# Optimization experiments

Measured on AMD Instinct MI355X. Metric: run time of the kernel, lower is better.

Reference implementation:

```python
import jax, jax.numpy as jnp
import numpy as np

N = 50000      # nodes
E = 400000     # edges
F_IN = 128     # num_features
HID = 64       # hidden_channels
HEADS = 4      # num_heads
HEADC = HID // HEADS  # 16
C = 10         # num_classes
K_HOPS = 2     # K
CST = 1e-05


def setup_inputs() -> dict:
    key = jax.random.key(0)
    ks = jax.random.split(key, 12)
    def lin(k, out_dim, in_dim):
        return jax.random.normal(k, (out_dim, in_dim), jnp.float32) / np.sqrt(in_dim).astype(np.float32)
    return {
        "node_feat": jax.random.normal(ks[0], (N, F_IN), jnp.float32),
        "edge_index": jax.random.randint(ks[1], (2, E), 0, N, jnp.int64),
        "W_in": lin(ks[2], HID, F_IN),   "b_in": jnp.zeros((HID,), jnp.float32),
        "W_q": lin(ks[3], HEADS * HEADC, HID), "b_q": jnp.zeros((HEADS * HEADC,), jnp.float32),
        "W_k": lin(ks[4], HEADS * HEADC, HID), "b_k": jnp.zeros((HEADS * HEADC,), jnp.float32),
        "W_v": lin(ks[5], HEADS * C, HID),     "b_v": jnp.zeros((HEADS * C,), jnp.float32),
        "W_out": lin(ks[6], C, HEADS * C),     "b_out": jnp.zeros((C,), jnp.float32),
        "hopwise": jnp.ones((K_HOPS + 1,), jnp.float32),
        "headwise": jnp.zeros((HEADS, K_HOPS), jnp.float32),
    }


def reference(node_feat, edge_index, W_in, b_in, W_q, b_q, W_k, b_k, W_v, b_v,
              W_out, b_out, hopwise, headwise):
    # input transform (dropout is identity in eval mode)
    x = jax.nn.relu(node_feat @ W_in.T + b_in)                       # [N, HID]
    Q = (1.0 + jax.nn.elu(x @ W_q.T + b_q)).reshape(N, HEADS, HEADC)  # [N,H,hc]
    Kf = (1.0 + jax.nn.elu(x @ W_k.T + b_k)).reshape(N, HEADS, HEADC)
    V = (x @ W_v.T + b_v).reshape(N, HEADS, C)                        # [N,H,C]

    M = jnp.einsum('nhi,nhj->nhij', Kf, V)                            # [N,H,hc,C]
    hidden = V * hopwise[0]                                           # gamma_softmax path
    layerwise = jax.nn.softmax(headwise, axis=0)                      # softmax over heads

    row, col = edge_index[0], edge_index[1]
    for hop in range(K_HOPS):
        # propM / propK: sum-aggregate source features into targets
        M = jax.ops.segment_sum(M[row], col, num_segments=N)
        Kf = jax.ops.segment_sum(Kf[row], col, num_segments=N)
        H = jnp.einsum('nhi,nhij->nhj', Q, M)                         # [N,H,C]
        Cd = jnp.einsum('nhi,nhi->nh', Q, Kf)[..., None] + CST        # [N,H,1]
        gamma = hopwise[hop + 1] * layerwise[:, hop][:, None]         # [H,1]
        hidden = hidden + gamma * (H / Cd)

    # multi_concat output projection
    out = hidden.reshape(N, HEADS * C) @ W_out.T + b_out              # [N,C]
    return out
```

## Files before the change

kernel.cpp:

```cpp
#include <hip/hip_runtime.h>
#include <hip/hip_bf16.h>

#define N_NODES 50000
#define N_EDGES 400000
#define F_IN    128
#define HID     64
#define HEADS   4
#define HEADC   16
#define C_CLS   10
#define HC      (HEADS * C_CLS)
#define CST     1e-5f

#define WIN_OFF 0
#define WQ_OFF  1024
#define WK_OFF  1536
#define WV_OFF  2048
#define WB_TOT  2432

typedef short bf16x8 __attribute__((ext_vector_type(8)));
typedef float f32x4  __attribute__((ext_vector_type(4)));
typedef float floatx2 __attribute__((ext_vector_type(2)));

__device__ __forceinline__ unsigned pack_bf16x2(float a, float b) {
    union { __hip_bfloat162 h2; unsigned u; } cv;
    cv.h2.x = __float2bfloat16(a);
    cv.h2.y = __float2bfloat16(b);
    return cv.u;
}
__device__ __forceinline__ float2 bf2_to_f2(unsigned u) {
    union { unsigned x; float f; } a, b;
    a.x = u << 16;
    b.x = u & 0xffff0000u;
    return make_float2(a.f, b.f);
}
union FragU { uint4 u; bf16x8 b; };
__device__ __forceinline__ bf16x8 ldfrag(const uint4* p) { FragU f; f.u = *p; return f.b; }
__device__ __forceinline__ bf16x8 pack8(const float4& a0, const float4& a1) {
    FragU f;
    f.u.x = pack_bf16x2(a0.x, a0.y);
    f.u.y = pack_bf16x2(a0.z, a0.w);
    f.u.z = pack_bf16x2(a1.x, a1.y);
    f.u.w = pack_bf16x2(a1.z, a1.w);
    return f.b;
}
__device__ __forceinline__ void acc_edge_fp8(float kf, uint4 v, float* accM) {
    floatx2 f;
    f = __builtin_amdgcn_cvt_pk_f32_fp8(v.x, false); accM[0] += kf * f[0]; accM[1] += kf * f[1];
    f = __builtin_amdgcn_cvt_pk_f32_fp8(v.x, true);  accM[2] += kf * f[0]; accM[3] += kf * f[1];
    f = __builtin_amdgcn_cvt_pk_f32_fp8(v.y, false); accM[4] += kf * f[0]; accM[5] += kf * f[1];
    f = __builtin_amdgcn_cvt_pk_f32_fp8(v.y, true);  accM[6] += kf * f[0]; accM[7] += kf * f[1];
    f = __builtin_amdgcn_cvt_pk_f32_fp8(v.z, false); accM[8] += kf * f[0]; accM[9] += kf * f[1];
}

__global__ __launch_bounds__(256) void prep_kernel(
    const float* __restrict__ W_in, const float* __restrict__ W_q,
    const float* __restrict__ W_k,  const float* __restrict__ W_v,
    uint4* __restrict__ WB)
{
    const int idx = blockIdx.x * 256 + threadIdx.x;
    if (idx >= WB_TOT) return;
    const int lane = idx & 63;
    const int c = lane & 15, g = lane >> 4;
    const float* src = nullptr;
    if (idx < WQ_OFF) {
        const int f = idx >> 6, nt = f >> 2, kt = f & 3;
        src = W_in + (size_t)(nt * 16 + c) * F_IN + kt * 32 + g * 8;
    } else if (idx < WK_OFF) {
        const int f = (idx - WQ_OFF) >> 6, nt = f >> 1, kt = f & 1;
        src = W_q + (size_t)(nt * 16 + c) * HID + kt * 32 + g * 8;
    } else if (idx < WV_OFF) {
        const int f = (idx - WK_OFF) >> 6, nt = f >> 1, kt = f & 1;
        src = W_k + (size_t)(nt * 16 + c) * HID + kt * 32 + g * 8;
    } else {
        const int f = (idx - WV_OFF) >> 6, nt = f >> 1, kt = f & 1;
        const int row = nt * 16 + c;
        src = (row < HC) ? (W_v + (size_t)row * HID + kt * 32 + g * 8) : nullptr;
    }
    float v[8];
    #pragma unroll
    for (int j = 0; j < 8; ++j) v[j] = src ? src[j] : 0.0f;
    uint4 o;
    o.x = pack_bf16x2(v[0], v[1]);
    o.y = pack_bf16x2(v[2], v[3]);
    o.z = pack_bf16x2(v[4], v[5]);
    o.w = pack_bf16x2(v[6], v[7]);
    WB[idx] = o;
}

__global__ __launch_bounds__(256) void proj_kernel(
    const float* __restrict__ feat, const uint4* __restrict__ WB,
    const float* __restrict__ b_in, const float* __restrict__ b_q,
    const float* __restrict__ b_k,  const float* __restrict__ b_v,
    float* __restrict__ Q, __hip_bfloat16* __restrict__ Kf0,
    __hip_bfloat16* __restrict__ V0p)
{
    const int w = threadIdx.x >> 6;
    const int l = threadIdx.x & 63;
    const int c = l & 15, g = l >> 4;
    const int nb = blockIdx.x * 64 + w * 16;
    __shared__ float xs[4][16][68];

    f32x4 acc[4];
    #pragma unroll
    for (int nt = 0; nt < 4; ++nt) acc[nt] = (f32x4){0.f, 0.f, 0.f, 0.f};
    int arow = nb + c; if (arow >= N_NODES) arow = N_NODES - 1;
    const float* fbase = feat + (size_t)arow * F_IN + g * 8;
    #pragma unroll
    for (int kt = 0; kt < 4; ++kt) {
        const float4 a0 = *(const float4*)(fbase + kt * 32);
        const float4 a1 = *(const float4*)(fbase + kt * 32 + 4);
        const bf16x8 af = pack8(a0, a1);
        #pragma unroll
        for (int nt = 0; nt < 4; ++nt)
            acc[nt] = __builtin_amdgcn_mfma_f32_16x16x32_bf16(
                af, ldfrag(WB + WIN_OFF + (nt * 4 + kt) * 64 + l), acc[nt], 0, 0, 0);
    }
    #pragma unroll
    for (int nt = 0; nt < 4; ++nt) {
        const int col = nt * 16 + c;
        const float bi = b_in[col];
        #pragma unroll
        for (int i = 0; i < 4; ++i)
            xs[w][g * 4 + i][col] = fmaxf(acc[nt][i] + bi, 0.f);
    }
    __syncthreads();

    f32x4 qa[4], ka[4], va[3];
    #pragma unroll
    for (int nt = 0; nt < 4; ++nt) { qa[nt] = (f32x4){0.f,0.f,0.f,0.f}; ka[nt] = qa[nt]; }
    #pragma unroll
    for (int nt = 0; nt < 3; ++nt) va[nt] = (f32x4){0.f,0.f,0.f,0.f};
    #pragma unroll
    for (int kt = 0; kt < 2; ++kt) {
        const float* xr = &xs[w][c][kt * 32 + g * 8];
        const float4 x0 = *(const float4*)xr;
        const float4 x1 = *(const float4*)(xr + 4);
        const bf16x8 af = pack8(x0, x1);
        #pragma unroll
        for (int nt = 0; nt < 4; ++nt) {
            qa[nt] = __builtin_amdgcn_mfma_f32_16x16x32_bf16(
                af, ldfrag(WB + WQ_OFF + (nt * 2 + kt) * 64 + l), qa[nt], 0, 0, 0);
            ka[nt] = __builtin_amdgcn_mfma_f32_16x16x32_bf16(
                af, ldfrag(WB + WK_OFF + (nt * 2 + kt) * 64 + l), ka[nt], 0, 0, 0);
        }
        #pragma unroll
        for (int nt = 0; nt < 3; ++nt)
            va[nt] = __builtin_amdgcn_mfma_f32_16x16x32_bf16(
                af, ldfrag(WB + WV_OFF + (nt * 2 + kt) * 64 + l), va[nt], 0, 0, 0);
    }

    #pragma unroll
    for (int nt = 0; nt < 4; ++nt) {
        const int col = nt * 16 + c;
        const float bq = b_q[col], bk = b_k[col];
        #pragma unroll
        for (int i = 0; i < 4; ++i) {
            const int node = nb + g * 4 + i;
            if (node < N_NODES) {
                const float zq = qa[nt][i] + bq;
                Q[(size_t)node * HID + col] = (zq > 0.f) ? (zq + 1.f) : expf(zq);
                const float zk = ka[nt][i] + bk;
                Kf0[(size_t)node * HID + col] =
                    __float2bfloat16((zk > 0.f) ? (zk + 1.f) : expf(zk));
            }
        }
    }
    #pragma unroll
    for (int nt = 0; nt < 3; ++nt) {
        const int col = nt * 16 + c;
        if (col < HC) {
            const int hh = col / C_CLS, jj = col - hh * C_CLS;
            const float bv = b_v[col];
            #pragma unroll
            for (int i = 0; i < 4; ++i) {
                const int node = nb + g * 4 + i;
                if (node < N_NODES)
                    V0p[(size_t)node * 64 + hh * 16 + jj] = __float2bfloat16(va[nt][i] + bv);
            }
        }
    }
}

__global__ __launch_bounds__(256) void vconv_kernel(
    const __hip_bfloat16* __restrict__ V0p, uint4* __restrict__ V0f)
{
    const int t = blockIdx.x * 256 + threadIdx.x;
    if (t >= N_NODES * 4) return;
    const uint4* src = (const uint4*)V0p + (size_t)t * 2;
    const uint4 a = src[0];
    const unsigned b0 = ((const unsigned*)(src + 1))[0];
    float v[10];
    float2 f;
    f = bf2_to_f2(a.x); v[0] = f.x; v[1] = f.y;
    f = bf2_to_f2(a.y); v[2] = f.x; v[3] = f.y;
    f = bf2_to_f2(a.z); v[4] = f.x; v[5] = f.y;
    f = bf2_to_f2(a.w); v[6] = f.x; v[7] = f.y;
    f = bf2_to_f2(b0);  v[8] = f.x; v[9] = f.y;
    int d0 = 0, d1 = 0, d2 = 0;
    d0 = __builtin_amdgcn_cvt_pk_fp8_f32(v[0], v[1], d0, false);
    d0 = __builtin_amdgcn_cvt_pk_fp8_f32(v[2], v[3], d0, true);
    d1 = __builtin_amdgcn_cvt_pk_fp8_f32(v[4], v[5], d1, false);
    d1 = __builtin_amdgcn_cvt_pk_fp8_f32(v[6], v[7], d1, true);
    d2 = __builtin_amdgcn_cvt_pk_fp8_f32(v[8], v[9], d2, false);
    uint4 o;
    o.x = (unsigned)d0; o.y = (unsigned)d1; o.z = (unsigned)d2; o.w = 0u;
    V0f[t] = o;
}

__global__ __launch_bounds__(256) void hist_kernel(
    const int* __restrict__ ecol, int* __restrict__ deg)
{
    const int e = blockIdx.x * 256 + threadIdx.x;
    if (e < N_EDGES) atomicAdd(&deg[ecol[e]], 1);
}

__global__ __launch_bounds__(256) void offsets_kernel(
    const int* __restrict__ deg, int* __restrict__ rowptr,
    int* __restrict__ cursor, int* __restrict__ gcount)
{
    const int t    = threadIdx.x;
    const int lane = t & 63;
    const int wid  = t >> 6;
    const int n    = blockIdx.x * 256 + t;
    const int d    = (n < N_NODES) ? deg[n] : 0;

    int x = d;
    #pragma unroll
    for (int off = 1; off < 64; off <<= 1) {
        int v = __shfl_up(x, off);
        x += (lane >= off) ? v : 0;
    }

    __shared__ int wsum[4];
    __shared__ int wbase[4];
    __shared__ int bbase;
    if (lane == 63) wsum[wid] = x;
    __syncthreads();
    if (t == 0) {
        int b = 0;
        #pragma unroll
        for (int w = 0; w < 4; ++w) { wbase[w] = b; b += wsum[w]; }
        bbase = atomicAdd(gcount, b);
    }
    __syncthreads();

    if (n < N_NODES) {
        const int excl = bbase + wbase[wid] + (x - d);
        rowptr[n] = excl;
        cursor[n] = excl;
    }
}

__global__ __launch_bounds__(256) void scatter_kernel(
    const int* __restrict__ erow, const int* __restrict__ ecol,
    int* __restrict__ cursor, int* __restrict__ csr_src)
{
    const int e = blockIdx.x * 256 + threadIdx.x;
    if (e < N_EDGES) {
        const int pos = atomicAdd(&cursor[ecol[e]], 1);
        csr_src[pos] = erow[e];
    }
}

__global__ __launch_bounds__(256) void hop1_gather(
    const int* __restrict__ csr_src, const int* __restrict__ rowptr,
    const int* __restrict__ deg,
    const float* __restrict__ Q, const __hip_bfloat16* __restrict__ Kf0,
    const uint4* __restrict__ V0f,
    uint2* __restrict__ M1a, unsigned* __restrict__ M1b,
    float* __restrict__ H1, float* __restrict__ Cd1)
{
    const int sub  = threadIdx.x >> 6;
    const int lane = threadIdx.x & 63;
    const int n    = blockIdx.x * 4 + sub;
    if (n >= N_NODES) return;
    const int h = lane >> 4;
    const int r = lane & 15;

    float accM[C_CLS];
    #pragma unroll
    for (int j = 0; j < C_CLS; ++j) accM[j] = 0.0f;
    float accK = 0.0f;

    const int beg = rowptr[n];
    const int d   = deg[n];
    int e = 0;
    for (; e + 8 <= d; e += 8) {
        int s[8];
        #pragma unroll
        for (int i = 0; i < 8; ++i) s[i] = csr_src[beg + e + i];
        float kf[8];
        uint4 vv[8];
        #pragma unroll
        for (int i = 0; i < 8; ++i) {
            kf[i] = __bfloat162float(Kf0[(size_t)s[i] * HID + lane]);
            vv[i] = V0f[(size_t)s[i] * 4 + h];
        }
        #pragma unroll
        for (int i = 0; i < 8; ++i) accK += kf[i];
        #pragma unroll
        for (int i = 0; i < 8; ++i) acc_edge_fp8(kf[i], vv[i], accM);
    }
    for (; e + 4 <= d; e += 4) {
        int s[4];
        #pragma unroll
        for (int i = 0; i < 4; ++i) s[i] = csr_src[beg + e + i];
        float kf[4];
        uint4 vv[4];
        #pragma unroll
        for (int i = 0; i < 4; ++i) {
            kf[i] = __bfloat162float(Kf0[(size_t)s[i] * HID + lane]);
            vv[i] = V0f[(size_t)s[i] * 4 + h];
        }
        #pragma unroll
        for (int i = 0; i < 4; ++i) accK += kf[i];
        #pragma unroll
        for (int i = 0; i < 4; ++i) acc_edge_fp8(kf[i], vv[i], accM);
    }
    for (; e < d; ++e) {
        const int ss = csr_src[beg + e];
        const float kf = __bfloat162float(Kf0[(size_t)ss * HID + lane]);
        const uint4 vv0 = V0f[(size_t)ss * 4 + h];
        accK += kf;
        acc_edge_fp8(kf, vv0, accM);
    }

    int d0 = 0, d1 = 0, d2 = 0;
    d0 = __builtin_amdgcn_cvt_pk_fp8_f32(accM[0], accM[1], d0, false);
    d0 = __builtin_amdgcn_cvt_pk_fp8_f32(accM[2], accM[3], d0, true);
    d1 = __builtin_amdgcn_cvt_pk_fp8_f32(accM[4], accM[5], d1, false);
    d1 = __builtin_amdgcn_cvt_pk_fp8_f32(accM[6], accM[7], d1, true);
    d2 = __builtin_amdgcn_cvt_pk_fp8_f32(accM[8], accM[9], d2, false);
    uint2 sa; sa.x = (unsigned)d0; sa.y = (unsigned)d1;
    M1a[(size_t)n * 64 + lane] = sa;
    M1b[(size_t)n * 64 + lane] =
        ((unsigned)d2 & 0xFFFFu) | (pack_bf16x2(0.f, accK) & 0xFFFF0000u);

    const float q = Q[(size_t)n * HID + lane];
    float pc = q * accK;
    pc += __shfl_xor(pc, 1);
    pc += __shfl_xor(pc, 2);
    pc += __shfl_xor(pc, 4);
    pc += __shfl_xor(pc, 8);
    if (r == 0) Cd1[(size_t)n * HEADS + h] = pc;

    float pj[C_CLS];
    #pragma unroll
    for (int j = 0; j < C_CLS; ++j) {
        pj[j] = q * accM[j];
        pj[j] += __shfl_xor(pj[j], 1);
        pj[j] += __shfl_xor(pj[j], 2);
        pj[j] += __shfl_xor(pj[j], 4);
        pj[j] += __shfl_xor(pj[j], 8);
    }
    if (r < C_CLS) {
        float val = 0.0f;
        #pragma unroll
        for (int j = 0; j < C_CLS; ++j) val = (r == j) ? pj[j] : val;
        H1[(size_t)n * HC + h * C_CLS + r] = val;
    }
}

__global__ __launch_bounds__(256) void hop2_gather(
    const int* __restrict__ csr_src, const int* __restrict__ rowptr,
    const int* __restrict__ deg,
    const float* __restrict__ Q,
    const uint2* __restrict__ M1a, const unsigned* __restrict__ M1b,
    float* __restrict__ H2, float* __restrict__ Cd2)
{
    const int sub  = threadIdx.x >> 6;
    const int lane = threadIdx.x & 63;
    const int n    = blockIdx.x * 4 + sub;
    if (n >= N_NODES) return;
    const int h = lane >> 4;
    const int r = lane & 15;

    const float q = Q[(size_t)n * HID + lane];
    float accM[C_CLS];
    #pragma unroll
    for (int j = 0; j < C_CLS; ++j) accM[j] = 0.0f;
    float accK = 0.0f;

    const int beg = rowptr[n];
    const int d   = deg[n];
    int e = 0;
    for (; e + 4 <= d; e += 4) {
        int s[4];
        #pragma unroll
        for (int i = 0; i < 4; ++i) s[i] = csr_src[beg + e + i];
        uint2 wa[4];
        unsigned wb[4];
        #pragma unroll
        for (int i = 0; i < 4; ++i) {
            wa[i] = M1a[(size_t)s[i] * 64 + lane];
            wb[i] = M1b[(size_t)s[i] * 64 + lane];
        }
        #pragma unroll
        for (int i = 0; i < 4; ++i) {
            accK += bf2_to_f2(wb[i]).y;
            floatx2 f;
            f = __builtin_amdgcn_cvt_pk_f32_fp8(wa[i].x, false); accM[0] += f[0]; accM[1] += f[1];
            f = __builtin_amdgcn_cvt_pk_f32_fp8(wa[i].x, true);  accM[2] += f[0]; accM[3] += f[1];
            f = __builtin_amdgcn_cvt_pk_f32_fp8(wa[i].y, false); accM[4] += f[0]; accM[5] += f[1];
            f = __builtin_amdgcn_cvt_pk_f32_fp8(wa[i].y, true);  accM[6] += f[0]; accM[7] += f[1];
            f = __builtin_amdgcn_cvt_pk_f32_fp8(wb[i], false);   accM[8] += f[0]; accM[9] += f[1];
        }
    }
    for (; e < d; ++e) {
        const int ss = csr_src[beg + e];
        const uint2 wa0 = M1a[(size_t)ss * 64 + lane];
        const unsigned wb0 = M1b[(size_t)ss * 64 + lane];
        accK += bf2_to_f2(wb0).y;
        floatx2 f;
        f = __builtin_amdgcn_cvt_pk_f32_fp8(wa0.x, false); accM[0] += f[0]; accM[1] += f[1];
        f = __builtin_amdgcn_cvt_pk_f32_fp8(wa0.x, true);  accM[2] += f[0]; accM[3] += f[1];
        f = __builtin_amdgcn_cvt_pk_f32_fp8(wa0.y, false); accM[4] += f[0]; accM[5] += f[1];
        f = __builtin_amdgcn_cvt_pk_f32_fp8(wa0.y, true);  accM[6] += f[0]; accM[7] += f[1];
        f = __builtin_amdgcn_cvt_pk_f32_fp8(wb0, false);   accM[8] += f[0]; accM[9] += f[1];
    }

    float pc = q * accK;
    pc += __shfl_xor(pc, 1);
    pc += __shfl_xor(pc, 2);
    pc += __shfl_xor(pc, 4);
    pc += __shfl_xor(pc, 8);
    if (r == 0) Cd2[(size_t)n * HEADS + h] = pc;

    float pj[C_CLS];
    #pragma unroll
    for (int j = 0; j < C_CLS; ++j) {
        pj[j] = q * accM[j];
        pj[j] += __shfl_xor(pj[j], 1);
        pj[j] += __shfl_xor(pj[j], 2);
        pj[j] += __shfl_xor(pj[j], 4);
        pj[j] += __shfl_xor(pj[j], 8);
    }
    if (r < C_CLS) {
        float val = 0.0f;
        #pragma unroll
        for (int j = 0; j < C_CLS; ++j) val = (r == j) ? pj[j] : val;
        H2[(size_t)n * HC + h * C_CLS + r] = val;
    }
}

__global__ __launch_bounds__(256) void combine_kernel(
    const __hip_bfloat16* __restrict__ V0p,
    const float* __restrict__ H1, const float* __restrict__ Cd1,
    const float* __restrict__ H2, const float* __restrict__ Cd2,
    const float* __restrict__ hopwise, const float* __restrict__ headwise,
    const float* __restrict__ W_out, const float* __restrict__ b_out,
    float* __restrict__ out)
{
    const int n = blockIdx.x * blockDim.x + threadIdx.x;
    if (n >= N_NODES) return;

    float hv[HEADS][2];
    float m0 = -1e30f, m1 = -1e30f;
    #pragma unroll
    for (int h = 0; h < HEADS; ++h) {
        hv[h][0] = headwise[h * 2 + 0];
        hv[h][1] = headwise[h * 2 + 1];
        m0 = fmaxf(m0, hv[h][0]);
        m1 = fmaxf(m1, hv[h][1]);
    }
    float s0 = 0.0f, s1 = 0.0f;
    float e0[HEADS], e1[HEADS];
    #pragma unroll
    for (int h = 0; h < HEADS; ++h) {
        e0[h] = expf(hv[h][0] - m0); s0 += e0[h];
        e1[h] = expf(hv[h][1] - m1); s1 += e1[h];
    }
    const float hw0 = hopwise[0];
    float g1[HEADS], g2[HEADS];
    #pragma unroll
    for (int h = 0; h < HEADS; ++h) {
        g1[h] = hopwise[1] * e0[h] / s0;
        g2[h] = hopwise[2] * e1[h] / s1;
    }

    float hidden[HC];
    #pragma unroll
    for (int h = 0; h < HEADS; ++h) {
        const float icd1 = 1.0f / (Cd1[(size_t)n * HEADS + h] + CST);
        const float icd2 = 1.0f / (Cd2[(size_t)n * HEADS + h] + CST);
        #pragma unroll
        for (int j = 0; j < C_CLS; ++j) {
            const int idx = h * C_CLS + j;
            hidden[idx] = hw0 * __bfloat162float(V0p[(size_t)n * 64 + h * 16 + j])
                        + g1[h] * H1[(size_t)n * HC + idx] * icd1
                        + g2[h] * H2[(size_t)n * HC + idx] * icd2;
        }
    }

    #pragma unroll
    for (int c = 0; c < C_CLS; ++c) {
        float acc = b_out[c];
        const float* w = W_out + c * HC;
        #pragma unroll
        for (int k = 0; k < HC; ++k) acc += w[k] * hidden[k];
        out[(size_t)n * C_CLS + c] = acc;
    }
}

extern "C" void kernel_launch(void* const* d_in, const int* in_sizes, int n_in,
                              void* d_out, int out_size, void* d_ws, size_t ws_size,
                              hipStream_t stream)
{
    const float* feat     = (const float*)d_in[0];
    const int*   eidx     = (const int*)  d_in[1];
    const float* W_in     = (const float*)d_in[2];
    const float* b_in     = (const float*)d_in[3];
    const float* W_q      = (const float*)d_in[4];
    const float* b_q      = (const float*)d_in[5];
    const float* W_k      = (const float*)d_in[6];
    const float* b_k      = (const float*)d_in[7];
    const float* W_v      = (const float*)d_in[8];
    const float* b_v      = (const float*)d_in[9];
    const float* W_out    = (const float*)d_in[10];
    const float* b_out    = (const float*)d_in[11];
    const float* hopwise  = (const float*)d_in[12];
    const float* headwise = (const float*)d_in[13];
    float* out = (float*)d_out;

    const int* erow = eidx;
    const int* ecol = eidx + N_EDGES;

    float* ws = (float*)d_ws;
    size_t off = 0;
    float* Q    = ws + off; off += (size_t)N_NODES * HID;
    __hip_bfloat16* Kf0 = (__hip_bfloat16*)(ws + off); off += (size_t)N_NODES * HID / 2;
    __hip_bfloat16* V0p = (__hip_bfloat16*)(ws + off); off += (size_t)N_NODES * 32;
    uint4* V0f = (uint4*)(ws + off); off += (size_t)N_NODES * 16;
    uint2* M1a = (uint2*)(ws + off); off += (size_t)N_NODES * 128;
    unsigned* M1b = (unsigned*)(ws + off); off += (size_t)N_NODES * 64;
    float* H1   = ws + off; off += (size_t)N_NODES * HC;
    float* Cd1  = ws + off; off += (size_t)N_NODES * HEADS;
    float* H2   = ws + off; off += (size_t)N_NODES * HC;
    float* Cd2  = ws + off; off += (size_t)N_NODES * HEADS;
    uint4* WB   = (uint4*)(ws + off); off += (size_t)WB_TOT * 4;
    int* iws = (int*)(ws + off);
    int* deg     = iws;
    int* gcount  = iws + N_NODES;
    int* rowptr  = iws + N_NODES + 1;
    int* cursor  = iws + 2 * N_NODES + 1;
    int* csr_src = iws + 3 * N_NODES + 1;

    hipMemsetAsync(deg, 0, (N_NODES + 1) * sizeof(int), stream);

    prep_kernel<<<(WB_TOT + 255) / 256, 256, 0, stream>>>(W_in, W_q, W_k, W_v, WB);

    proj_kernel<<<(N_NODES + 63) / 64, 256, 0, stream>>>(
        feat, WB, b_in, b_q, b_k, b_v, Q, Kf0, V0p);

    vconv_kernel<<<(N_NODES * 4 + 255) / 256, 256, 0, stream>>>(V0p, V0f);

    hist_kernel<<<(N_EDGES + 255) / 256, 256, 0, stream>>>(ecol, deg);
    offsets_kernel<<<(N_NODES + 255) / 256, 256, 0, stream>>>(deg, rowptr, cursor, gcount);
    scatter_kernel<<<(N_EDGES + 255) / 256, 256, 0, stream>>>(erow, ecol, cursor, csr_src);

    hop1_gather<<<(N_NODES + 3) / 4, 256, 0, stream>>>(
        csr_src, rowptr, deg, Q, Kf0, V0f, M1a, M1b, H1, Cd1);

    hop2_gather<<<(N_NODES + 3) / 4, 256, 0, stream>>>(
        csr_src, rowptr, deg, Q, M1a, M1b, H2, Cd2);

    combine_kernel<<<(N_NODES + 255) / 256, 256, 0, stream>>>(
        V0p, H1, Cd1, H2, Cd2, hopwise, headwise, W_out, b_out, out);
}
```

Baseline: 187.8 us.

## Fuse V fp8 conversion into projection and preload CSR indices via readlane

The separate vconv kernel is removed. The projection kernel now stages V values through shared memory and writes both the bf16 and the fp8 copies of V directly. Both hop gather kernels load up to 64 neighbor indices with one coalesced per-lane read, then broadcast them with readlane. This replaces the repeated scalar index loads inside the edge loops. The changes save a kernel launch, one round trip of V through memory, and index-load latency, at the cost of an extra __syncthreads and a fallback path for degrees above 64.

```diff
diff --git a/kernel.cpp b/kernel.cpp
--- a/kernel.cpp
+++ b/kernel.cpp
@@ -50,6 +50,14 @@
     f = __builtin_amdgcn_cvt_pk_f32_fp8(v.y, false); accM[4] += kf * f[0]; accM[5] += kf * f[1];
     f = __builtin_amdgcn_cvt_pk_f32_fp8(v.y, true);  accM[6] += kf * f[0]; accM[7] += kf * f[1];
     f = __builtin_amdgcn_cvt_pk_f32_fp8(v.z, false); accM[8] += kf * f[0]; accM[9] += kf * f[1];
+}
+__device__ __forceinline__ void acc_edge_fp8_plain(uint4 v, float* accM) {
+    floatx2 f;
+    f = __builtin_amdgcn_cvt_pk_f32_fp8(v.x, false); accM[0] += f[0]; accM[1] += f[1];
+    f = __builtin_amdgcn_cvt_pk_f32_fp8(v.x, true);  accM[2] += f[0]; accM[3] += f[1];
+    f = __builtin_amdgcn_cvt_pk_f32_fp8(v.y, false); accM[4] += f[0]; accM[5] += f[1];
+    f = __builtin_amdgcn_cvt_pk_f32_fp8(v.y, true);  accM[6] += f[0]; accM[7] += f[1];
+    f = __builtin_amdgcn_cvt_pk_f32_fp8(v.z, false); accM[8] += f[0]; accM[9] += f[1];
 }
 
 __global__ __launch_bounds__(256) void prep_kernel(
@@ -92,7 +100,7 @@
     const float* __restrict__ b_in, const float* __restrict__ b_q,
     const float* __restrict__ b_k,  const float* __restrict__ b_v,
     float* __restrict__ Q, __hip_bfloat16* __restrict__ Kf0,
-    __hip_bfloat16* __restrict__ V0p)
+    __hip_bfloat16* __restrict__ V0p, uint4* __restrict__ V0f)
 {
     const int w = threadIdx.x >> 6;
     const int l = threadIdx.x & 63;
@@ -165,46 +173,45 @@
             }
         }
     }
+
     #pragma unroll
     for (int nt = 0; nt < 3; ++nt) {
         const int col = nt * 16 + c;
         if (col < HC) {
-            const int hh = col / C_CLS, jj = col - hh * C_CLS;
             const float bv = b_v[col];
             #pragma unroll
-            for (int i = 0; i < 4; ++i) {
-                const int node = nb + g * 4 + i;
-                if (node < N_NODES)
-                    V0p[(size_t)node * 64 + hh * 16 + jj] = __float2bfloat16(va[nt][i] + bv);
-            }
+            for (int i = 0; i < 4; ++i)
+                xs[w][g * 4 + i][col] = va[nt][i] + bv;
         }
     }
-}
-
-__global__ __launch_bounds__(256) void vconv_kernel(
-    const __hip_bfloat16* __restrict__ V0p, uint4* __restrict__ V0f)
-{
-    const int t = blockIdx.x * 256 + threadIdx.x;
-    if (t >= N_NODES * 4) return;
-    const uint4* src = (const uint4*)V0p + (size_t)t * 2;
-    const uint4 a = src[0];
-    const unsigned b0 = ((const unsigned*)(src + 1))[0];
-    float v[10];
-    float2 f;
-    f = bf2_to_f2(a.x); v[0] = f.x; v[1] = f.y;
-    f = bf2_to_f2(a.y); v[2] = f.x; v[3] = f.y;
-    f = bf2_to_f2(a.z); v[4] = f.x; v[5] = f.y;
-    f = bf2_to_f2(a.w); v[6] = f.x; v[7] = f.y;
-    f = bf2_to_f2(b0);  v[8] = f.x; v[9] = f.y;
-    int d0 = 0, d1 = 0, d2 = 0;
-    d0 = __builtin_amdgcn_cvt_pk_fp8_f32(v[0], v[1], d0, false);
-    d0 = __builtin_amdgcn_cvt_pk_fp8_f32(v[2], v[3], d0, true);
-    d1 = __builtin_amdgcn_cvt_pk_fp8_f32(v[4], v[5], d1, false);
-    d1 = __builtin_amdgcn_cvt_pk_fp8_f32(v[6], v[7], d1, true);
-    d2 = __builtin_amdgcn_cvt_pk_fp8_f32(v[8], v[9], d2, false);
-    uint4 o;
-    o.x = (unsigned)d0; o.y = (unsigned)d1; o.z = (unsigned)d2; o.w = 0u;
-    V0f[t] = o;
+    __syncthreads();
+
+    {
+        const int nl = l >> 2, hh = l & 3;
+        const int node = nb + nl;
+        float v[10];
+        #pragma unroll
+        for (int j = 0; j < 10; ++j) v[j] = xs[w][nl][hh * 10 + j];
+        if (node < N_NODES) {
+            unsigned p0 = pack_bf16x2(v[0], v[1]);
+            unsigned p1 = pack_bf16x2(v[2], v[3]);
+            unsigned p2 = pack_bf16x2(v[4], v[5]);
+            unsigned p3 = pack_bf16x2(v[6], v[7]);
+            unsigned p4 = pack_bf16x2(v[8], v[9]);
+            unsigned* dst = (unsigned*)(V0p + (size_t)node * 64 + hh * 16);
+            uint4 o; o.x = p0; o.y = p1; o.z = p2; o.w = p3;
+            *(uint4*)dst = o;
+            dst[4] = p4;
+            int d0 = 0, d1 = 0, d2 = 0;
+            d0 = __builtin_amdgcn_cvt_pk_fp8_f32(v[0], v[1], d0, false);
+            d0 = __builtin_amdgcn_cvt_pk_fp8_f32(v[2], v[3], d0, true);
+            d1 = __builtin_amdgcn_cvt_pk_fp8_f32(v[4], v[5], d1, false);
+            d1 = __builtin_amdgcn_cvt_pk_fp8_f32(v[6], v[7], d1, true);
+            d2 = __builtin_amdgcn_cvt_pk_fp8_f32(v[8], v[9], d2, false);
+            uint4 f8; f8.x = (unsigned)d0; f8.y = (unsigned)d1; f8.z = (unsigned)d2; f8.w = 0u;
+            V0f[(size_t)node * 4 + hh] = f8;
+        }
+    }
 }
 
 __global__ __launch_bounds__(256) void hist_kernel(
@@ -284,45 +291,43 @@
 
     const int beg = rowptr[n];
     const int d   = deg[n];
+    const int dc  = (d < 64) ? d : 64;
+    int sreg = 0;
+    if (lane < dc) sreg = csr_src[beg + lane];
+
     int e = 0;
-    for (; e + 8 <= d; e += 8) {
-        int s[8];
-        #pragma unroll
-        for (int i = 0; i < 8; ++i) s[i] = csr_src[beg + e + i];
-        float kf[8];
-        uint4 vv[8];
-        #pragma unroll
-        for (int i = 0; i < 8; ++i) {
-            kf[i] = __bfloat162float(Kf0[(size_t)s[i] * HID + lane]);
-            vv[i] = V0f[(size_t)s[i] * 4 + h];
-        }
-        #pragma unroll
-        for (int i = 0; i < 8; ++i) accK += kf[i];
-        #pragma unroll
-        for (int i = 0; i < 8; ++i) acc_edge_fp8(kf[i], vv[i], accM);
-    }
-    for (; e + 4 <= d; e += 4) {
-        int s[4];
-        #pragma unroll
-        for (int i = 0; i < 4; ++i) s[i] = csr_src[beg + e + i];
-        float kf[4];
-        uint4 vv[4];
-        #pragma unroll
-        for (int i = 0; i < 4; ++i) {
-            kf[i] = __bfloat162float(Kf0[(size_t)s[i] * HID + lane]);
-            vv[i] = V0f[(size_t)s[i] * 4 + h];
-        }
-        #pragma unroll
-        for (int i = 0; i < 4; ++i) accK += kf[i];
-        #pragma unroll
-        for (int i = 0; i < 4; ++i) acc_edge_fp8(kf[i], vv[i], accM);
+    for (; e + 4 <= dc; e += 4) {
+        const int s0 = __builtin_amdgcn_readlane(sreg, e);
+        const int s1 = __builtin_amdgcn_readlane(sreg, e + 1);
+        const int s2 = __builtin_amdgcn_readlane(sreg, e + 2);
+        const int s3 = __builtin_amdgcn_readlane(sreg, e + 3);
+        const float kf0 = __bfloat162float(Kf0[(size_t)s0 * HID + lane]);
+        const float kf1 = __bfloat162float(Kf0[(size_t)s1 * HID + lane]);
+        const float kf2 = __bfloat162float(Kf0[(size_t)s2 * HID + lane]);
+        const float kf3 = __bfloat162float(Kf0[(size_t)s3 * HID + lane]);
+        const uint4 v0 = V0f[(size_t)s0 * 4 + h];
+        const uint4 v1 = V0f[(size_t)s1 * 4 + h];
+        const uint4 v2 = V0f[(size_t)s2 * 4 + h];
+        const uint4 v3 = V0f[(size_t)s3 * 4 + h];
+        accK += (kf0 + kf1) + (kf2 + kf3);
+        acc_edge_fp8(kf0, v0, accM);
+        acc_edge_fp8(kf1, v1, accM);
+        acc_edge_fp8(kf2, v2, accM);
+        acc_edge_fp8(kf3, v3, accM);
+    }
+    for (; e < dc; ++e) {
+        const int s0 = __builtin_amdgcn_readlane(sreg, e);
+        const float kf = __bfloat162float(Kf0[(size_t)s0 * HID + lane]);
+        const uint4 v0 = V0f[(size_t)s0 * 4 + h];
+        accK += kf;
+        acc_edge_fp8(kf, v0, accM);
     }
     for (; e < d; ++e) {
-        const int ss = csr_src[beg + e];
-        const float kf = __bfloat162float(Kf0[(size_t)ss * HID + lane]);
-        const uint4 vv0 = V0f[(size_t)ss * 4 + h];
+        const int s0 = csr_src[beg + e];
+        const float kf = __bfloat162float(Kf0[(size_t)s0 * HID + lane]);
+        const uint4 v0 = V0f[(size_t)s0 * 4 + h];
         accK += kf;
-        acc_edge_fp8(kf, vv0, accM);
+        acc_edge_fp8(kf, v0, accM);
     }
 
     int d0 = 0, d1 = 0, d2 = 0;
@@ -383,40 +388,46 @@
 
     const int beg = rowptr[n];
     const int d   = deg[n];
+    const int dc  = (d < 64) ? d : 64;
+    int sreg = 0;
+    if (lane < dc) sreg = csr_src[beg + lane];
+
     int e = 0;
-    for (; e + 4 <= d; e += 4) {
-        int s[4];
-        #pragma unroll
-        for (int i = 0; i < 4; ++i) s[i] = csr_src[beg + e + i];
-        uint2 wa[4];
-        unsigned wb[4];
-        #pragma unroll
-        for (int i = 0; i < 4; ++i) {
-            wa[i] = M1a[(size_t)s[i] * 64 + lane];
-            wb[i] = M1b[(size_t)s[i] * 64 + lane];
-        }
-        #pragma unroll
-        for (int i = 0; i < 4; ++i) {
-            accK += bf2_to_f2(wb[i]).y;
-            floatx2 f;
-            f = __builtin_amdgcn_cvt_pk_f32_fp8(wa[i].x, false); accM[0] += f[0]; accM[1] += f[1];
-            f = __builtin_amdgcn_cvt_pk_f32_fp8(wa[i].x, true);  accM[2] += f[0]; accM[3] += f[1];
-            f = __builtin_amdgcn_cvt_pk_f32_fp8(wa[i].y, false); accM[4] += f[0]; accM[5] += f[1];
-            f = __builtin_amdgcn_cvt_pk_f32_fp8(wa[i].y, true);  accM[6] += f[0]; accM[7] += f[1];
-            f = __builtin_amdgcn_cvt_pk_f32_fp8(wb[i], false);   accM[8] += f[0]; accM[9] += f[1];
-        }
+    for (; e + 4 <= dc; e += 4) {
+        const int s0 = __builtin_amdgcn_readlane(sreg, e);
+        const int s1 = __builtin_amdgcn_readlane(sreg, e + 1);
+        const int s2 = __builtin_amdgcn_readlane(sreg, e + 2);
+        const int s3 = __builtin_amdgcn_readlane(sreg, e + 3);
+        const uint2 a0 = M1a[(size_t)s0 * 64 + lane];
+        const uint2 a1 = M1a[(size_t)s1 * 64 + lane];
+        const uint2 a2 = M1a[(size_t)s2 * 64 + lane];
+        const uint2 a3 = M1a[(size_t)s3 * 64 + lane];
+        const unsigned b0 = M1b[(size_t)s0 * 64 + lane];
+        const unsigned b1 = M1b[(size_t)s1 * 64 + lane];
+        const unsigned b2 = M1b[(size_t)s2 * 64 + lane];
+        const unsigned b3 = M1b[(size_t)s3 * 64 + lane];
+        accK += bf2_to_f2(b0).y + bf2_to_f2(b1).y + bf2_to_f2(b2).y + bf2_to_f2(b3).y;
+        uint4 w;
+        w.x = a0.x; w.y = a0.y; w.z = b0; acc_edge_fp8_plain(w, accM);
+        w.x = a1.x; w.y = a1.y; w.z = b1; acc_edge_fp8_plain(w, accM);
+        w.x = a2.x; w.y = a2.y; w.z = b2; acc_edge_fp8_plain(w, accM);
+        w.x = a3.x; w.y = a3.y; w.z = b3; acc_edge_fp8_plain(w, accM);
+    }
+    for (; e < dc; ++e) {
+        const int s0 = __builtin_amdgcn_readlane(sreg, e);
+        const uint2 a0 = M1a[(size_t)s0 * 64 + lane];
+        const unsigned b0 = M1b[(size_t)s0 * 64 + lane];
+        accK += bf2_to_f2(b0).y;
+        uint4 w; w.x = a0.x; w.y = a0.y; w.z = b0;
+        acc_edge_fp8_plain(w, accM);
     }
     for (; e < d; ++e) {
-        const int ss = csr_src[beg + e];
-        const uint2 wa0 = M1a[(size_t)ss * 64 + lane];
-        const unsigned wb0 = M1b[(size_t)ss * 64 + lane];
-        accK += bf2_to_f2(wb0).y;
-        floatx2 f;
-        f = __builtin_amdgcn_cvt_pk_f32_fp8(wa0.x, false); accM[0] += f[0]; accM[1] += f[1];
-        f = __builtin_amdgcn_cvt_pk_f32_fp8(wa0.x, true);  accM[2] += f[0]; accM[3] += f[1];
-        f = __builtin_amdgcn_cvt_pk_f32_fp8(wa0.y, false); accM[4] += f[0]; accM[5] += f[1];
-        f = __builtin_amdgcn_cvt_pk_f32_fp8(wa0.y, true);  accM[6] += f[0]; accM[7] += f[1];
-        f = __builtin_amdgcn_cvt_pk_f32_fp8(wb0, false);   accM[8] += f[0]; accM[9] += f[1];
+        const int s0 = csr_src[beg + e];
+        const uint2 a0 = M1a[(size_t)s0 * 64 + lane];
+        const unsigned b0 = M1b[(size_t)s0 * 64 + lane];
+        accK += bf2_to_f2(b0).y;
+        uint4 w; w.x = a0.x; w.y = a0.y; w.z = b0;
+        acc_edge_fp8_plain(w, accM);
     }
 
     float pc = q * accK;
@@ -550,9 +561,7 @@
     prep_kernel<<<(WB_TOT + 255) / 256, 256, 0, stream>>>(W_in, W_q, W_k, W_v, WB);
 
     proj_kernel<<<(N_NODES + 63) / 64, 256, 0, stream>>>(
-        feat, WB, b_in, b_q, b_k, b_v, Q, Kf0, V0p);
-
-    vconv_kernel<<<(N_NODES * 4 + 255) / 256, 256, 0, stream>>>(V0p, V0f);
+        feat, WB, b_in, b_q, b_k, b_v, Q, Kf0, V0p, V0f);
 
     hist_kernel<<<(N_EDGES + 255) / 256, 256, 0, stream>>>(ecol, deg);
     offsets_kernel<<<(N_NODES + 255) / 256, 256, 0, stream>>>(deg, rowptr, cursor, gcount);
```

After: 171.1 us, median of 2. 8.9% less time.
